# Performance work log

Hardware: AMD Instinct MI355X
Metric: run time of the kernel (lower is better)

Reference implementation:

```python
import jax, jax.numpy as jnp
import numpy as np

ALPHA_LEAKY = 0.2
NUM_LAYERS = 3
N, D = 8192, 64


def setup_inputs() -> dict:
    key = jax.random.key(0)
    ks = jax.random.split(key, 7)
    return {
        "X": jax.random.normal(ks[0], (N, D), dtype=jnp.float32),
        "A": jax.random.uniform(ks[1], (N, N), dtype=jnp.float32),
        "Ws": jax.random.normal(ks[2], (NUM_LAYERS, D, D), dtype=jnp.float32) * 0.1,
        "bWs": jax.random.normal(ks[3], (NUM_LAYERS, D), dtype=jnp.float32) * 0.1,
        "a1": jax.random.normal(ks[4], (NUM_LAYERS, D), dtype=jnp.float32) * 0.1,
        "a2": jax.random.normal(ks[5], (NUM_LAYERS, D), dtype=jnp.float32) * 0.1,
        "ba": jax.random.normal(ks[6], (NUM_LAYERS,), dtype=jnp.float32) * 0.1,
    }


def reference(X, A, Ws, bWs, a1, a2, ba):
    # Note: original torch code computes A_hat/D_inv_sqrt from A but never
    # uses them; A only provides shape, so it does not affect the output.
    n = X.shape[0]
    A_MAS = jnp.ones((n, n), dtype=X.dtype)
    for l in range(NUM_LAYERS):
        Wh = X @ Ws[l].T + bWs[l]                      # (N, D)
        # att Linear on cat([Wh_i, Wh_j]) decomposes: e_ij = f1_i + f2_j + b
        f1 = Wh @ a1[l]                                # (N,)
        f2 = Wh @ a2[l]                                # (N,)
        e = f1[:, None] + f2[None, :] + ba[l]          # (N, N)
        e = jnp.where(e > 0, e, ALPHA_LEAKY * e)       # leaky relu
        alpha = jax.nn.softmax(e, axis=1)              # row softmax over j
        A_MAS = A_MAS * alpha
    return A_MAS @ X                                    # (N, D)
```

## Files before the change

kernel.cpp:

```cpp
#include <hip/hip_runtime.h>

#define NN 8192
#define DD 64
#define NL 3
#define LOG2E 1.4426950408889634f

typedef _Float16 f16x8 __attribute__((ext_vector_type(8)));
typedef _Float16 f16x2 __attribute__((ext_vector_type(2)));
typedef float f32x2 __attribute__((ext_vector_type(2)));
typedef float f32x16 __attribute__((ext_vector_type(16)));

union F16U { f16x8 v8; f16x2 h2[4]; };

__global__ __launch_bounds__(256) void mas_prep(const float* __restrict__ X,
                                                const float* __restrict__ Ws,
                                                const float* __restrict__ bWs,
                                                const float* __restrict__ a1,
                                                const float* __restrict__ a2,
                                                const float* __restrict__ ba,
                                                float* __restrict__ Rt,
                                                _Float16* __restrict__ E2h,
                                                _Float16* __restrict__ E2sh,
                                                _Float16* __restrict__ Xf) {
    if (blockIdx.x < 96) {
        const int l = blockIdx.x >> 5;
        const int i = ((blockIdx.x & 31) << 8) + threadIdx.x;

        float xr[DD];
        const float4* X4 = (const float4*)(X + (size_t)i * DD);
#pragma unroll
        for (int q = 0; q < DD / 4; ++q) {
            float4 v = X4[q];
            xr[4 * q + 0] = v.x; xr[4 * q + 1] = v.y;
            xr[4 * q + 2] = v.z; xr[4 * q + 3] = v.w;
        }

        const float* W   = Ws  + l * DD * DD;
        const float* a1l = a1  + l * DD;
        const float* a2l = a2  + l * DD;
        const float* bwl = bWs + l * DD;

        float f1 = 0.f, f2 = 0.f;
#pragma unroll 4
        for (int d = 0; d < DD; ++d) {
            float wh = bwl[d];
            const float* wr = W + d * DD;
#pragma unroll
            for (int k = 0; k < DD; ++k) wh = fmaf(xr[k], wr[k], wh);
            f1 = fmaf(wh, a1l[d], f1);
            f2 = fmaf(wh, a2l[d], f2);
        }
        const float a = (f1 + ba[l]) * LOG2E;
        const float b = f2 * LOG2E;
        Rt  [l * NN + i] = exp2f(-0.8f * a);
        E2h [l * NN + i] = (_Float16)exp2f(b - 4.0f);
        E2sh[l * NN + i] = (_Float16)exp2f(0.2f * b - 4.0f);
    } else {
        const int t = (blockIdx.x - 96) * 256 + threadIdx.x;
        const int lane = t & 63;
        const int st = t >> 6;
        const int S = st >> 1, tl = st & 1;
        const int d = tl * 32 + (lane & 31);
        const int j0 = S * 16 + (lane >> 5) * 8;
        f16x8 v;
#pragma unroll
        for (int e = 0; e < 8; ++e) v[e] = (_Float16)X[(size_t)(j0 + e) * DD + d];
        *(f16x8*)(Xf + (size_t)t * 8) = v;
    }
}

template <int USE_LDS>
__global__ __launch_bounds__(256, 4) void mas_main14(const _Float16* __restrict__ Xf,
                                                     const float* __restrict__ Rt,
                                                     const _Float16* __restrict__ E2h,
                                                     const _Float16* __restrict__ E2sh,
                                                     float* __restrict__ numpart,
                                                     float* __restrict__ zpart,
                                                     float* __restrict__ out,
                                                     int nqb) {
    __shared__ float red[4][64][33];
    __shared__ float zred[4][3][32];
    __shared__ float zfin[3][32];

    const int tid  = threadIdx.x;
    const int lane = tid & 63;
    const int wv   = tid >> 6;
    const int hi   = lane >> 5;
    const int row  = lane & 31;
    const int rt   = blockIdx.x;
    const int q    = blockIdx.y;
    const int i    = rt * 32 + row;

    const float r0f = Rt[0 * NN + i], r1f = Rt[1 * NN + i], r2f = Rt[2 * NN + i];
    const f16x2 R0p = {(_Float16)r0f, (_Float16)r0f};
    const f16x2 R1p = {(_Float16)r1f, (_Float16)r1f};
    const f16x2 R2p = {(_Float16)r2f, (_Float16)r2f};

    const int jspan = NN / nqb;
    const int wspan = jspan >> 2;
    const int jbase = q * jspan + wv * wspan;
    const int nst   = wspan >> 4;
    const int wvoff = wv * wspan;

    _Float16* tab = (_Float16*)&red[0][0][0];
    if (USE_LDS) {
        const int jblk = q * jspan;
        const _Float16* s0 = E2h  + 0 * NN + jblk;
        const _Float16* s1 = E2h  + 1 * NN + jblk;
        const _Float16* s2 = E2h  + 2 * NN + jblk;
        const _Float16* s3 = E2sh + 0 * NN + jblk;
        const _Float16* s4 = E2sh + 1 * NN + jblk;
        const _Float16* s5 = E2sh + 2 * NN + jblk;
        *(f16x8*)&tab[0 * 2048 + tid * 8] = *(const f16x8*)(s0 + tid * 8);
        *(f16x8*)&tab[1 * 2048 + tid * 8] = *(const f16x8*)(s1 + tid * 8);
        *(f16x8*)&tab[2 * 2048 + tid * 8] = *(const f16x8*)(s2 + tid * 8);
        *(f16x8*)&tab[3 * 2048 + tid * 8] = *(const f16x8*)(s3 + tid * 8);
        *(f16x8*)&tab[4 * 2048 + tid * 8] = *(const f16x8*)(s4 + tid * 8);
        *(f16x8*)&tab[5 * 2048 + tid * 8] = *(const f16x8*)(s5 + tid * 8);
        __syncthreads();
    }

    const _Float16* q20 = E2h  + 0 * NN + jbase + hi * 8;
    const _Float16* q21 = E2h  + 1 * NN + jbase + hi * 8;
    const _Float16* q22 = E2h  + 2 * NN + jbase + hi * 8;
    const _Float16* r20 = E2sh + 0 * NN + jbase + hi * 8;
    const _Float16* r21 = E2sh + 1 * NN + jbase + hi * 8;
    const _Float16* r22 = E2sh + 2 * NN + jbase + hi * 8;
    const f16x8* pB = (const f16x8*)Xf + (size_t)(jbase >> 4) * 128 + lane;

    const int tloc0 = wvoff + hi * 8;

    f32x16 acc0 = {};
    f32x16 acc1 = {};
    f32x2 z0p = {0.f, 0.f}, z1p = {0.f, 0.f}, z2p = {0.f, 0.f};

    for (int s = 0; s < nst; ++s) {
        const int o = s * 16;
        F16U g0, g1, g2, h0, h1, h2v;
        if (USE_LDS) {
            const int t0 = tloc0 + o;
            g0.v8  = *(const f16x8*)&tab[0 * 2048 + t0];
            g1.v8  = *(const f16x8*)&tab[1 * 2048 + t0];
            g2.v8  = *(const f16x8*)&tab[2 * 2048 + t0];
            h0.v8  = *(const f16x8*)&tab[3 * 2048 + t0];
            h1.v8  = *(const f16x8*)&tab[4 * 2048 + t0];
            h2v.v8 = *(const f16x8*)&tab[5 * 2048 + t0];
        } else {
            g0.v8  = *(const f16x8*)(q20 + o);
            g1.v8  = *(const f16x8*)(q21 + o);
            g2.v8  = *(const f16x8*)(q22 + o);
            h0.v8  = *(const f16x8*)(r20 + o);
            h1.v8  = *(const f16x8*)(r21 + o);
            h2v.v8 = *(const f16x8*)(r22 + o);
        }
        const f16x8 vb0 = pB[s * 128];
        const f16x8 vb1 = pB[s * 128 + 64];

        f16x2 m0[4], m1[4], m2[4];
#pragma unroll
        for (int g = 0; g < 4; ++g) {
            m0[g] = __builtin_elementwise_max(g0.h2[g],  R0p * h0.h2[g]);
            m1[g] = __builtin_elementwise_max(g1.h2[g],  R1p * h1.h2[g]);
            m2[g] = __builtin_elementwise_max(g2.h2[g],  R2p * h2v.h2[g]);
        }
        const f16x2 t0 = (m0[0] + m0[1]) + (m0[2] + m0[3]);
        const f16x2 t1 = (m1[0] + m1[1]) + (m1[2] + m1[3]);
        const f16x2 t2 = (m2[0] + m2[1]) + (m2[2] + m2[3]);
        z0p += (f32x2){(float)t0[0], (float)t0[1]};
        z1p += (f32x2){(float)t1[0], (float)t1[1]};
        z2p += (f32x2){(float)t2[0], (float)t2[1]};

        F16U wa;
#pragma unroll
        for (int g = 0; g < 4; ++g)
            wa.h2[g] = m0[g] * (m1[g] * m2[g]);

        acc0 = __builtin_amdgcn_mfma_f32_32x32x16_f16(wa.v8, vb0, acc0, 0, 0, 0);
        acc1 = __builtin_amdgcn_mfma_f32_32x32x16_f16(wa.v8, vb1, acc1, 0, 0, 0);
    }

    float z0 = z0p[0] + z0p[1];
    float z1 = z1p[0] + z1p[1];
    float z2 = z2p[0] + z2p[1];
    z0 += __shfl_xor(z0, 32);
    z1 += __shfl_xor(z1, 32);
    z2 += __shfl_xor(z2, 32);

    if (USE_LDS) __syncthreads();

#pragma unroll
    for (int g = 0; g < 4; ++g) {
        const int rb = 8 * g + 4 * hi;
        *(float4*)&red[wv][row][rb] =
            make_float4(acc0[4 * g], acc0[4 * g + 1], acc0[4 * g + 2], acc0[4 * g + 3]);
        *(float4*)&red[wv][row + 32][rb] =
            make_float4(acc1[4 * g], acc1[4 * g + 1], acc1[4 * g + 2], acc1[4 * g + 3]);
    }
    if (lane < 32) {
        zred[wv][0][row] = z0; zred[wv][1][row] = z1; zred[wv][2][row] = z2;
    }
    __syncthreads();

    if (tid < 96) {
        const int l = tid >> 5, r = tid & 31;
        const float Z = zred[0][l][r] + zred[1][l][r] + zred[2][l][r] + zred[3][l][r];
        if (nqb > 1) zpart[((size_t)q * 3 + l) * NN + rt * 32 + r] = Z;
        else zfin[l][r] = Z;
    }
    __syncthreads();

    {
        const int col = tid & 63;
        const int r0 = (tid >> 6) * 8;
        float s[8] = {0, 0, 0, 0, 0, 0, 0, 0};
#pragma unroll
        for (int w = 0; w < 4; ++w) {
            const float4 u = *(const float4*)&red[w][col][r0];
            const float4 v = *(const float4*)&red[w][col][r0 + 4];
            s[0] += u.x; s[1] += u.y; s[2] += u.z; s[3] += u.w;
            s[4] += v.x; s[5] += v.y; s[6] += v.z; s[7] += v.w;
        }
        if (nqb > 1) {
            float* np = numpart + ((size_t)q * NN + (size_t)rt * 32) * DD;
#pragma unroll
            for (int u2 = 0; u2 < 8; ++u2) np[(size_t)(r0 + u2) * DD + col] = s[u2];
        } else {
#pragma unroll
            for (int u2 = 0; u2 < 8; ++u2) {
                const int r = r0 + u2;
                const float inv = 1.0f / (zfin[0][r] * (zfin[1][r] * zfin[2][r]));
                out[(size_t)(rt * 32 + r) * DD + col] = s[u2] * inv;
            }
        }
    }
}

__global__ __launch_bounds__(256) void mas_comb14(const float* __restrict__ numpart,
                                                  const float* __restrict__ zpart,
                                                  float* __restrict__ out, int nqb) {
    const int idx = blockIdx.x * 256 + threadIdx.x;
    const int i = idx >> 6;
    float s = 0.f;
    for (int q = 0; q < nqb; ++q) s += numpart[(size_t)q * NN * DD + idx];
    float Z0 = 0.f, Z1 = 0.f, Z2 = 0.f;
    for (int q = 0; q < nqb; ++q) {
        Z0 += zpart[((size_t)q * 3 + 0) * NN + i];
        Z1 += zpart[((size_t)q * 3 + 1) * NN + i];
        Z2 += zpart[((size_t)q * 3 + 2) * NN + i];
    }
    out[idx] = s / (Z0 * (Z1 * Z2));
}

extern "C" void kernel_launch(void* const* d_in, const int* in_sizes, int n_in,
                              void* d_out, int out_size, void* d_ws, size_t ws_size,
                              hipStream_t stream) {
    const float* X   = (const float*)d_in[0];
    const float* Ws  = (const float*)d_in[2];
    const float* bWs = (const float*)d_in[3];
    const float* a1  = (const float*)d_in[4];
    const float* a2  = (const float*)d_in[5];
    const float* ba  = (const float*)d_in[6];
    float* out = (float*)d_out;

    float* Rt = (float*)d_ws;
    _Float16* E2h  = (_Float16*)(Rt + NL * NN);
    _Float16* E2sh = E2h + NL * NN;
    _Float16* Xf   = E2sh + NL * NN;

    const size_t fixed = (size_t)NL * NN * 4 + (size_t)(2 * NL * NN) * 2
                       + (size_t)NN * DD * 2;
    const size_t per_q = (size_t)NN * DD * 4 + (size_t)NL * NN * 4;
    int nqb = 1;
    if (ws_size >= fixed + 4 * per_q) nqb = 4;
    else if (ws_size >= fixed + 2 * per_q) nqb = 2;

    float* numpart = (float*)(Xf + (size_t)NN * DD);
    float* zpart   = numpart + (size_t)nqb * NN * DD;

    mas_prep<<<352, 256, 0, stream>>>(X, Ws, bWs, a1, a2, ba, Rt, E2h, E2sh, Xf);
    dim3 grid(NN / 32, nqb);
    if (nqb == 4)
        mas_main14<1><<<grid, 256, 0, stream>>>(Xf, Rt, E2h, E2sh,
                                                numpart, zpart, out, nqb);
    else
        mas_main14<0><<<grid, 256, 0, stream>>>(Xf, Rt, E2h, E2sh,
                                                numpart, zpart, out, nqb);
    if (nqb > 1)
        mas_comb14<<<NN * DD / 256, 256, 0, stream>>>(numpart, zpart, out, nqb);
}
```

Measured before the change: 56.40 us.

## Replace split-K partial sums and combine kernel with 1024-thread single-pass blocks

The main kernel now uses 1024-thread blocks (16 waves) per 32-row tile and walks all 8192 columns in LDS-staged chunks of 2048, instead of splitting columns across 4 blocks and merging partials in a separate combine kernel. The cross-wave numerator and normalizer reductions happen in shared memory, and the output is written normalized directly. This removes the partial-sum global traffic and one kernel launch. In exchange the grid drops to 256 blocks, with two barriers per chunk that may stall waves.

Measured after the change: 55.02 us. -2.5%, faster.

```diff
diff --git a/kernel.cpp b/kernel.cpp
--- a/kernel.cpp
+++ b/kernel.cpp
@@ -4,6 +4,8 @@
 #define DD 64
 #define NL 3
 #define LOG2E 1.4426950408889634f
+#define CHUNK 2048
+#define NCHUNK (NN / CHUNK)
 
 typedef _Float16 f16x8 __attribute__((ext_vector_type(8)));
 typedef _Float16 f16x2 __attribute__((ext_vector_type(2)));
@@ -69,18 +71,16 @@
     }
 }
 
-template <int USE_LDS>
-__global__ __launch_bounds__(256, 4) void mas_main14(const _Float16* __restrict__ Xf,
-                                                     const float* __restrict__ Rt,
-                                                     const _Float16* __restrict__ E2h,
-                                                     const _Float16* __restrict__ E2sh,
-                                                     float* __restrict__ numpart,
-                                                     float* __restrict__ zpart,
-                                                     float* __restrict__ out,
-                                                     int nqb) {
-    __shared__ float red[4][64][33];
-    __shared__ float zred[4][3][32];
-    __shared__ float zfin[3][32];
+__global__ __launch_bounds__(1024, 4) void mas_main16(const _Float16* __restrict__ Xf,
+                                                      const float* __restrict__ Rt,
+                                                      const _Float16* __restrict__ E2h,
+                                                      const _Float16* __restrict__ E2sh,
+                                                      float* __restrict__ out) {
+    __shared__ float smem[18528];
+    _Float16* tab = (_Float16*)smem;
+    float (*red)[64][33] = (float(*)[64][33])smem;
+    float* zredf = smem + 16896;
+    float* zfin  = smem + 18432;
 
     const int tid  = threadIdx.x;
     const int lane = tid & 63;
@@ -88,7 +88,6 @@
     const int hi   = lane >> 5;
     const int row  = lane & 31;
     const int rt   = blockIdx.x;
-    const int q    = blockIdx.y;
     const int i    = rt * 32 + row;
 
     const float r0f = Rt[0 * NN + i], r1f = Rt[1 * NN + i], r2f = Rt[2 * NN + i];
@@ -96,87 +95,67 @@
     const f16x2 R1p = {(_Float16)r1f, (_Float16)r1f};
     const f16x2 R2p = {(_Float16)r2f, (_Float16)r2f};
 
-    const int jspan = NN / nqb;
-    const int wspan = jspan >> 2;
-    const int jbase = q * jspan + wv * wspan;
-    const int nst   = wspan >> 4;
-    const int wvoff = wv * wspan;
-
-    _Float16* tab = (_Float16*)&red[0][0][0];
-    if (USE_LDS) {
-        const int jblk = q * jspan;
-        const _Float16* s0 = E2h  + 0 * NN + jblk;
-        const _Float16* s1 = E2h  + 1 * NN + jblk;
-        const _Float16* s2 = E2h  + 2 * NN + jblk;
-        const _Float16* s3 = E2sh + 0 * NN + jblk;
-        const _Float16* s4 = E2sh + 1 * NN + jblk;
-        const _Float16* s5 = E2sh + 2 * NN + jblk;
-        *(f16x8*)&tab[0 * 2048 + tid * 8] = *(const f16x8*)(s0 + tid * 8);
-        *(f16x8*)&tab[1 * 2048 + tid * 8] = *(const f16x8*)(s1 + tid * 8);
-        *(f16x8*)&tab[2 * 2048 + tid * 8] = *(const f16x8*)(s2 + tid * 8);
-        *(f16x8*)&tab[3 * 2048 + tid * 8] = *(const f16x8*)(s3 + tid * 8);
-        *(f16x8*)&tab[4 * 2048 + tid * 8] = *(const f16x8*)(s4 + tid * 8);
-        *(f16x8*)&tab[5 * 2048 + tid * 8] = *(const f16x8*)(s5 + tid * 8);
-        __syncthreads();
-    }
-
-    const _Float16* q20 = E2h  + 0 * NN + jbase + hi * 8;
-    const _Float16* q21 = E2h  + 1 * NN + jbase + hi * 8;
-    const _Float16* q22 = E2h  + 2 * NN + jbase + hi * 8;
-    const _Float16* r20 = E2sh + 0 * NN + jbase + hi * 8;
-    const _Float16* r21 = E2sh + 1 * NN + jbase + hi * 8;
-    const _Float16* r22 = E2sh + 2 * NN + jbase + hi * 8;
-    const f16x8* pB = (const f16x8*)Xf + (size_t)(jbase >> 4) * 128 + lane;
-
-    const int tloc0 = wvoff + hi * 8;
-
     f32x16 acc0 = {};
     f32x16 acc1 = {};
     f32x2 z0p = {0.f, 0.f}, z1p = {0.f, 0.f}, z2p = {0.f, 0.f};
 
-    for (int s = 0; s < nst; ++s) {
-        const int o = s * 16;
-        F16U g0, g1, g2, h0, h1, h2v;
-        if (USE_LDS) {
-            const int t0 = tloc0 + o;
-            g0.v8  = *(const f16x8*)&tab[0 * 2048 + t0];
-            g1.v8  = *(const f16x8*)&tab[1 * 2048 + t0];
-            g2.v8  = *(const f16x8*)&tab[2 * 2048 + t0];
-            h0.v8  = *(const f16x8*)&tab[3 * 2048 + t0];
-            h1.v8  = *(const f16x8*)&tab[4 * 2048 + t0];
-            h2v.v8 = *(const f16x8*)&tab[5 * 2048 + t0];
-        } else {
-            g0.v8  = *(const f16x8*)(q20 + o);
-            g1.v8  = *(const f16x8*)(q21 + o);
-            g2.v8  = *(const f16x8*)(q22 + o);
-            h0.v8  = *(const f16x8*)(r20 + o);
-            h1.v8  = *(const f16x8*)(r21 + o);
-            h2v.v8 = *(const f16x8*)(r22 + o);
-        }
-        const f16x8 vb0 = pB[s * 128];
-        const f16x8 vb1 = pB[s * 128 + 64];
-
-        f16x2 m0[4], m1[4], m2[4];
-#pragma unroll
-        for (int g = 0; g < 4; ++g) {
-            m0[g] = __builtin_elementwise_max(g0.h2[g],  R0p * h0.h2[g]);
-            m1[g] = __builtin_elementwise_max(g1.h2[g],  R1p * h1.h2[g]);
-            m2[g] = __builtin_elementwise_max(g2.h2[g],  R2p * h2v.h2[g]);
-        }
-        const f16x2 t0 = (m0[0] + m0[1]) + (m0[2] + m0[3]);
-        const f16x2 t1 = (m1[0] + m1[1]) + (m1[2] + m1[3]);
-        const f16x2 t2 = (m2[0] + m2[1]) + (m2[2] + m2[3]);
-        z0p += (f32x2){(float)t0[0], (float)t0[1]};
-        z1p += (f32x2){(float)t1[0], (float)t1[1]};
-        z2p += (f32x2){(float)t2[0], (float)t2[1]};
-
-        F16U wa;
-#pragma unroll
-        for (int g = 0; g < 4; ++g)
-            wa.h2[g] = m0[g] * (m1[g] * m2[g]);
-
-        acc0 = __builtin_amdgcn_mfma_f32_32x32x16_f16(wa.v8, vb0, acc0, 0, 0, 0);
-        acc1 = __builtin_amdgcn_mfma_f32_32x32x16_f16(wa.v8, vb1, acc1, 0, 0, 0);
+    for (int c = 0; c < NCHUNK; ++c) {
+        const int jc = c * CHUNK;
+        {
+            const int fv = tid;
+            const int st = fv >> 8, v = fv & 255;
+            const _Float16* base = (st < 3) ? (E2h + st * NN + jc)
+                                            : (E2sh + (st - 3) * NN + jc);
+            *(f16x8*)&tab[st * CHUNK + v * 8] = *(const f16x8*)(base + v * 8);
+            if (tid < 512) {
+                const int fv2 = tid + 1024;
+                const int st2 = fv2 >> 8, v2 = fv2 & 255;
+                const _Float16* base2 = (st2 < 3) ? (E2h + st2 * NN + jc)
+                                                  : (E2sh + (st2 - 3) * NN + jc);
+                *(f16x8*)&tab[st2 * CHUNK + v2 * 8] = *(const f16x8*)(base2 + v2 * 8);
+            }
+        }
+        __syncthreads();
+
+        const int o0 = wv * (CHUNK / 16) + hi * 8;
+        const f16x8* pBc = (const f16x8*)Xf
+                         + ((size_t)(jc >> 4) + (size_t)wv * 8) * 128 + lane;
+
+#pragma unroll
+        for (int s = 0; s < 8; ++s) {
+            const int o = o0 + s * 16;
+            F16U g0, g1, g2, h0, h1, h2v;
+            g0.v8  = *(const f16x8*)&tab[0 * CHUNK + o];
+            g1.v8  = *(const f16x8*)&tab[1 * CHUNK + o];
+            g2.v8  = *(const f16x8*)&tab[2 * CHUNK + o];
+            h0.v8  = *(const f16x8*)&tab[3 * CHUNK + o];
+            h1.v8  = *(const f16x8*)&tab[4 * CHUNK + o];
+            h2v.v8 = *(const f16x8*)&tab[5 * CHUNK + o];
+            const f16x8 vb0 = pBc[s * 128];
+            const f16x8 vb1 = pBc[s * 128 + 64];
+
+            f16x2 m0[4], m1[4], m2[4];
+#pragma unroll
+            for (int g = 0; g < 4; ++g) {
+                m0[g] = __builtin_elementwise_max(g0.h2[g], R0p * h0.h2[g]);
+                m1[g] = __builtin_elementwise_max(g1.h2[g], R1p * h1.h2[g]);
+                m2[g] = __builtin_elementwise_max(g2.h2[g], R2p * h2v.h2[g]);
+            }
+            const f16x2 t0 = (m0[0] + m0[1]) + (m0[2] + m0[3]);
+            const f16x2 t1 = (m1[0] + m1[1]) + (m1[2] + m1[3]);
+            const f16x2 t2 = (m2[0] + m2[1]) + (m2[2] + m2[3]);
+            z0p += (f32x2){(float)t0[0], (float)t0[1]};
+            z1p += (f32x2){(float)t1[0], (float)t1[1]};
+            z2p += (f32x2){(float)t2[0], (float)t2[1]};
+
+            F16U wa;
+#pragma unroll
+            for (int g = 0; g < 4; ++g) wa.h2[g] = m0[g] * (m1[g] * m2[g]);
+
+            acc0 = __builtin_amdgcn_mfma_f32_32x32x16_f16(wa.v8, vb0, acc0, 0, 0, 0);
+            acc1 = __builtin_amdgcn_mfma_f32_32x32x16_f16(wa.v8, vb1, acc1, 0, 0, 0);
+        }
+        __syncthreads();
     }
 
     float z0 = z0p[0] + z0p[1];
@@ -185,70 +164,59 @@
     z0 += __shfl_xor(z0, 32);
     z1 += __shfl_xor(z1, 32);
     z2 += __shfl_xor(z2, 32);
-
-    if (USE_LDS) __syncthreads();
-
-#pragma unroll
-    for (int g = 0; g < 4; ++g) {
-        const int rb = 8 * g + 4 * hi;
-        *(float4*)&red[wv][row][rb] =
-            make_float4(acc0[4 * g], acc0[4 * g + 1], acc0[4 * g + 2], acc0[4 * g + 3]);
-        *(float4*)&red[wv][row + 32][rb] =
-            make_float4(acc1[4 * g], acc1[4 * g + 1], acc1[4 * g + 2], acc1[4 * g + 3]);
-    }
     if (lane < 32) {
-        zred[wv][0][row] = z0; zred[wv][1][row] = z1; zred[wv][2][row] = z2;
+        zredf[(wv * 3 + 0) * 32 + row] = z0;
+        zredf[(wv * 3 + 1) * 32 + row] = z1;
+        zredf[(wv * 3 + 2) * 32 + row] = z2;
+    }
+
+    if (wv < 8) {
+#pragma unroll
+        for (int g = 0; g < 4; ++g) {
+            const int rb = 8 * g + 4 * hi;
+            *(float4*)&red[wv][row][rb] =
+                make_float4(acc0[4*g], acc0[4*g+1], acc0[4*g+2], acc0[4*g+3]);
+            *(float4*)&red[wv][row + 32][rb] =
+                make_float4(acc1[4*g], acc1[4*g+1], acc1[4*g+2], acc1[4*g+3]);
+        }
+    }
+    __syncthreads();
+
+    if (wv >= 8) {
+        const int w8 = wv - 8;
+#pragma unroll
+        for (int g = 0; g < 4; ++g) {
+            const int rb = 8 * g + 4 * hi;
+            float4 u = *(float4*)&red[w8][row][rb];
+            u.x += acc0[4*g]; u.y += acc0[4*g+1]; u.z += acc0[4*g+2]; u.w += acc0[4*g+3];
+            *(float4*)&red[w8][row][rb] = u;
+            float4 v = *(float4*)&red[w8][row + 32][rb];
+            v.x += acc1[4*g]; v.y += acc1[4*g+1]; v.z += acc1[4*g+2]; v.w += acc1[4*g+3];
+            *(float4*)&red[w8][row + 32][rb] = v;
+        }
     }
     __syncthreads();
 
     if (tid < 96) {
         const int l = tid >> 5, r = tid & 31;
-        const float Z = zred[0][l][r] + zred[1][l][r] + zred[2][l][r] + zred[3][l][r];
-        if (nqb > 1) zpart[((size_t)q * 3 + l) * NN + rt * 32 + r] = Z;
-        else zfin[l][r] = Z;
+        float Z = 0.f;
+#pragma unroll
+        for (int w = 0; w < 16; ++w) Z += zredf[(w * 3 + l) * 32 + r];
+        zfin[l * 32 + r] = Z;
     }
     __syncthreads();
 
-    {
-        const int col = tid & 63;
-        const int r0 = (tid >> 6) * 8;
-        float s[8] = {0, 0, 0, 0, 0, 0, 0, 0};
-#pragma unroll
-        for (int w = 0; w < 4; ++w) {
-            const float4 u = *(const float4*)&red[w][col][r0];
-            const float4 v = *(const float4*)&red[w][col][r0 + 4];
-            s[0] += u.x; s[1] += u.y; s[2] += u.z; s[3] += u.w;
-            s[4] += v.x; s[5] += v.y; s[6] += v.z; s[7] += v.w;
-        }
-        if (nqb > 1) {
-            float* np = numpart + ((size_t)q * NN + (size_t)rt * 32) * DD;
-#pragma unroll
-            for (int u2 = 0; u2 < 8; ++u2) np[(size_t)(r0 + u2) * DD + col] = s[u2];
-        } else {
-#pragma unroll
-            for (int u2 = 0; u2 < 8; ++u2) {
-                const int r = r0 + u2;
-                const float inv = 1.0f / (zfin[0][r] * (zfin[1][r] * zfin[2][r]));
-                out[(size_t)(rt * 32 + r) * DD + col] = s[u2] * inv;
-            }
-        }
-    }
-}
-
-__global__ __launch_bounds__(256) void mas_comb14(const float* __restrict__ numpart,
-                                                  const float* __restrict__ zpart,
-                                                  float* __restrict__ out, int nqb) {
-    const int idx = blockIdx.x * 256 + threadIdx.x;
-    const int i = idx >> 6;
-    float s = 0.f;
-    for (int q = 0; q < nqb; ++q) s += numpart[(size_t)q * NN * DD + idx];
-    float Z0 = 0.f, Z1 = 0.f, Z2 = 0.f;
-    for (int q = 0; q < nqb; ++q) {
-        Z0 += zpart[((size_t)q * 3 + 0) * NN + i];
-        Z1 += zpart[((size_t)q * 3 + 1) * NN + i];
-        Z2 += zpart[((size_t)q * 3 + 2) * NN + i];
-    }
-    out[idx] = s / (Z0 * (Z1 * Z2));
+#pragma unroll
+    for (int p0 = 0; p0 < 2048; p0 += 1024) {
+        const int p = p0 + tid;
+        const int col = p & 63;
+        const int r = p >> 6;
+        float s = 0.f;
+#pragma unroll
+        for (int w = 0; w < 8; ++w) s += red[w][col][r];
+        const float inv = 1.0f / (zfin[0 * 32 + r] * (zfin[1 * 32 + r] * zfin[2 * 32 + r]));
+        out[(size_t)(rt * 32 + r) * DD + col] = s * inv;
+    }
 }
 
 extern "C" void kernel_launch(void* const* d_in, const int* in_sizes, int n_in,
@@ -267,24 +235,6 @@
     _Float16* E2sh = E2h + NL * NN;
     _Float16* Xf   = E2sh + NL * NN;
 
-    const size_t fixed = (size_t)NL * NN * 4 + (size_t)(2 * NL * NN) * 2
-                       + (size_t)NN * DD * 2;
-    const size_t per_q = (size_t)NN * DD * 4 + (size_t)NL * NN * 4;
-    int nqb = 1;
-    if (ws_size >= fixed + 4 * per_q) nqb = 4;
-    else if (ws_size >= fixed + 2 * per_q) nqb = 2;
-
-    float* numpart = (float*)(Xf + (size_t)NN * DD);
-    float* zpart   = numpart + (size_t)nqb * NN * DD;
-
     mas_prep<<<352, 256, 0, stream>>>(X, Ws, bWs, a1, a2, ba, Rt, E2h, E2sh, Xf);
-    dim3 grid(NN / 32, nqb);
-    if (nqb == 4)
-        mas_main14<1><<<grid, 256, 0, stream>>>(Xf, Rt, E2h, E2sh,
-                                                numpart, zpart, out, nqb);
-    else
-        mas_main14<0><<<grid, 256, 0, stream>>>(Xf, Rt, E2h, E2sh,
-                                                numpart, zpart, out, nqb);
-    if (nqb > 1)
-        mas_comb14<<<NN * DD / 256, 256, 0, stream>>>(numpart, zpart, out, nqb);
+    mas_main16<<<NN / 32, 1024, 0, stream>>>(Xf, Rt, E2h, E2sh, out);
 }
```
